# Kernel optimization log

Hardware: AMD Instinct MI355X
Metric: run time of the kernel (lower is better)

The kernel has to match this reference:

```python
import jax, jax.numpy as jnp
import numpy as np

QUANT_BLOCK = 32  # hardcoded in Linear8Bit


def setup_inputs() -> dict:
    key = jax.random.key(0)
    k1, k2, k3, k4, k5 = jax.random.split(key, 5)
    M, K, N = 64, 8192, 8192
    num_blocks = K // QUANT_BLOCK  # 256
    x = jax.random.normal(k1, (M, K), dtype=jnp.float32)
    scales = jax.random.uniform(k2, (num_blocks, N), dtype=jnp.float32, minval=0.001, maxval=0.02)
    zeros = jax.random.uniform(k3, (num_blocks, N), dtype=jnp.float32, minval=0.0, maxval=255.0)
    bias = jax.random.normal(k4, (N,), dtype=jnp.float32)
    quantized_weight = jax.random.randint(k5, (K, N), 0, 256, dtype=jnp.int32)
    return {"x": x, "scales": scales, "zeros": zeros, "bias": bias,
            "quantized_weight": quantized_weight}


def reference(x, scales, zeros, bias, quantized_weight):
    # The torch loop computes sum_b a_block @ (scale_b * (w_block - zero_b)),
    # which is exactly a full block-wise dequant followed by one matmul.
    K, N = quantized_weight.shape
    # Expand per-block scale/zero along K: [num_blocks, N] -> [K, N]
    scale_k = jnp.repeat(scales, QUANT_BLOCK, axis=0)[:K]
    zero_k = jnp.repeat(zeros, QUANT_BLOCK, axis=0)[:K]
    w_dq = scale_k * (quantized_weight.astype(jnp.float32) - zero_k)  # [K, N]
    out = jnp.matmul(x, w_dq) + bias  # [M, N]
    return out
```

## Files before the change

kernel.cpp:

```cpp
#include <hip/hip_runtime.h>

#define M_DIM 64
#define K_DIM 8192
#define N_DIM 8192
#define QB 32
#define NT 64
#define KC 64
#define SPLITS 4
#define KSPLIT (K_DIM / SPLITS)
#define NSTAGE (KSPLIT / KC)

typedef __attribute__((ext_vector_type(8))) short short8;
typedef __attribute__((ext_vector_type(8))) unsigned short ushort8;
typedef __attribute__((ext_vector_type(4))) float f32x4;
typedef __attribute__((ext_vector_type(4))) unsigned int u32x4;

static_assert(NSTAGE % 2 == 0 && NSTAGE * KC == KSPLIT, "tiling");

__device__ __forceinline__ unsigned short f2bf(float f) {
    unsigned u = __builtin_bit_cast(unsigned, f);
    u += 0x7fffu + ((u >> 16) & 1u);
    return (unsigned short)(u >> 16);
}

__global__ __launch_bounds__(256) void bias_init(const float* __restrict__ bias,
                                                 float* __restrict__ out) {
    int i = (blockIdx.x * 256 + threadIdx.x) * 4;
    *(f32x4*)(out + i) = *(const f32x4*)(bias + (i & (N_DIM - 1)));
}

__global__ __launch_bounds__(256) void xcvt(const float* __restrict__ x,
                                            unsigned short* __restrict__ xb) {
    int i = (blockIdx.x * 256 + threadIdx.x) * 8;
    f32x4 a = *(const f32x4*)(x + i);
    f32x4 b = *(const f32x4*)(x + i + 4);
    ushort8 o;
    #pragma unroll
    for (int e = 0; e < 4; ++e) { o[e] = f2bf(a[e]); o[4 + e] = f2bf(b[e]); }
    *(ushort8*)(xb + i) = o;
}

template <bool XBF>
__global__ __launch_bounds__(256, 2) void qgemm(
    const float* __restrict__ x,
    const unsigned short* __restrict__ xb,
    const float* __restrict__ scales,
    const float* __restrict__ zeros,
    const int*   __restrict__ qw,
    float*       __restrict__ out)
{
    __shared__ unsigned short lq[2][NT][72];
    __shared__ unsigned short lx[2][M_DIM][72];

    const int tid  = threadIdx.x;
    const int lane = tid & 63;
    const int w    = tid >> 6;

    const int n0 = blockIdx.x * NT;
    const int k0 = blockIdx.y * KSPLIT;

    const int qn   = n0 + lane;
    const int xrow = tid >> 2;
    const int xcol = (tid & 3) * 16;

    const int*   qp = qw     + (size_t)k0 * N_DIM + qn;
    const float* sp = scales + (size_t)(k0 >> 5) * N_DIM + qn;
    const float* zp = zeros  + (size_t)(k0 >> 5) * N_DIM + qn;

    int   qvA[16], qvB[16];
    float svA0, svA1, zvA0, zvA1, svB0, svB1, zvB0, zvB1;
    u32x4 xvA[2], xvB[2];
    f32x4 xfA[4], xfB[4];

#define LOADS(QV, S0, S1, Z0, Z1, XV, XF, T)                                  \
    do {                                                                      \
        const int* _p = qp + (size_t)(T) * KC * N_DIM;                        \
        _Pragma("unroll")                                                     \
        for (int s = 0; s < 4; ++s)                                           \
            _Pragma("unroll")                                                 \
            for (int j = 0; j < 4; ++j)                                       \
                QV[4 * s + j] = _p[(size_t)(16 * s + 4 * w + j) * N_DIM];     \
        S0 = sp[(size_t)(2 * (T)) * N_DIM];                                   \
        S1 = sp[(size_t)(2 * (T) + 1) * N_DIM];                               \
        Z0 = zp[(size_t)(2 * (T)) * N_DIM];                                   \
        Z1 = zp[(size_t)(2 * (T) + 1) * N_DIM];                               \
        if (XBF) {                                                            \
            const unsigned short* _xp =                                       \
                xb + (size_t)xrow * K_DIM + (k0 + (T) * KC) + xcol;           \
            XV[0] = *(const u32x4*)_xp;                                       \
            XV[1] = *(const u32x4*)(_xp + 8);                                 \
        } else {                                                              \
            const float* _xp =                                                \
                x + (size_t)xrow * K_DIM + (k0 + (T) * KC) + xcol;            \
            _Pragma("unroll")                                                 \
            for (int i = 0; i < 4; ++i) XF[i] = *(const f32x4*)(_xp + 4 * i); \
        }                                                                     \
    } while (0)

#define BODY(QV, S0, S1, Z0, Z1, XV, XF, CUR)                                 \
    do {                                                                      \
        const float _nz0 = -(S0) * (Z0), _nz1 = -(S1) * (Z1);                 \
        uint2 qd[4];                                                          \
        _Pragma("unroll")                                                     \
        for (int s = 0; s < 4; ++s) {                                         \
            const float _sc = (s < 2) ? (S0) : (S1);                          \
            const float _nz = (s < 2) ? _nz0 : _nz1;                          \
            unsigned short h0 = f2bf(fmaf((float)QV[4 * s + 0], _sc, _nz));   \
            unsigned short h1 = f2bf(fmaf((float)QV[4 * s + 1], _sc, _nz));   \
            unsigned short h2 = f2bf(fmaf((float)QV[4 * s + 2], _sc, _nz));   \
            unsigned short h3 = f2bf(fmaf((float)QV[4 * s + 3], _sc, _nz));   \
            qd[s].x = (unsigned)h0 | ((unsigned)h1 << 16);                    \
            qd[s].y = (unsigned)h2 | ((unsigned)h3 << 16);                    \
        }                                                                     \
        _Pragma("unroll")                                                     \
        for (int s = 0; s < 4; ++s)                                           \
            *(uint2*)&lq[CUR][lane][16 * s + 4 * w] = qd[s];                  \
        if (XBF) {                                                            \
            *(u32x4*)&lx[CUR][xrow][xcol]     = XV[0];                        \
            *(u32x4*)&lx[CUR][xrow][xcol + 8] = XV[1];                        \
        } else {                                                              \
            ushort8 xw0, xw1;                                                 \
            _Pragma("unroll")                                                 \
            for (int e = 0; e < 4; ++e) {                                     \
                xw0[e]     = f2bf(XF[0][e]);                                  \
                xw0[4 + e] = f2bf(XF[1][e]);                                  \
                xw1[e]     = f2bf(XF[2][e]);                                  \
                xw1[4 + e] = f2bf(XF[3][e]);                                  \
            }                                                                 \
            *(ushort8*)&lx[CUR][xrow][xcol]     = xw0;                        \
            *(ushort8*)&lx[CUR][xrow][xcol + 8] = xw1;                        \
        }                                                                     \
    } while (0)

#define MM(CUR)                                                               \
    do {                                                                      \
        _Pragma("unroll")                                                     \
        for (int c = 0; c < 2; ++c) {                                         \
            const short8 bf = *(const short8*)&lq[CUR][16 * w + (lane & 15)]  \
                                                 [32 * c + 8 * (lane >> 4)];  \
            _Pragma("unroll")                                                 \
            for (int r = 0; r < 4; ++r) {                                     \
                const short8 af = *(const short8*)&lx[CUR][16 * r + (lane & 15)] \
                                                     [32 * c + 8 * (lane >> 4)]; \
                acc[r] = __builtin_amdgcn_mfma_f32_16x16x32_bf16(af, bf, acc[r], 0, 0, 0); \
            }                                                                 \
        }                                                                     \
    } while (0)

    f32x4 acc[4];
    #pragma unroll
    for (int r = 0; r < 4; ++r) acc[r] = (f32x4){0.f, 0.f, 0.f, 0.f};

    LOADS(qvA, svA0, svA1, zvA0, zvA1, xvA, xfA, 0);

    for (int t = 0; t < NSTAGE; t += 2) {
        LOADS(qvB, svB0, svB1, zvB0, zvB1, xvB, xfB, t + 1);
        BODY(qvA, svA0, svA1, zvA0, zvA1, xvA, xfA, 0);
        __syncthreads();
        MM(0);
        if (t + 2 < NSTAGE)
            LOADS(qvA, svA0, svA1, zvA0, zvA1, xvA, xfA, t + 2);
        BODY(qvB, svB0, svB1, zvB0, zvB1, xvB, xfB, 1);
        __syncthreads();
        MM(1);
    }

#undef LOADS
#undef BODY
#undef MM

    const int cn = n0 + 16 * w + (lane & 15);
    #pragma unroll
    for (int r = 0; r < 4; ++r) {
        const int m = 16 * r + 4 * (lane >> 4);
        #pragma unroll
        for (int e = 0; e < 4; ++e)
            atomicAdd(out + (size_t)(m + e) * N_DIM + cn, acc[r][e]);
    }
}

extern "C" void kernel_launch(void* const* d_in, const int* in_sizes, int n_in,
                              void* d_out, int out_size, void* d_ws, size_t ws_size,
                              hipStream_t stream) {
    const float* x      = (const float*)d_in[0];
    const float* scales = (const float*)d_in[1];
    const float* zeros  = (const float*)d_in[2];
    const float* bias   = (const float*)d_in[3];
    const int*   qw     = (const int*)d_in[4];
    float* out = (float*)d_out;
    unsigned short* xbf = (unsigned short*)d_ws;

    const bool use_xbf = ws_size >= (size_t)M_DIM * K_DIM * 2;

    bias_init<<<dim3((M_DIM * N_DIM) / 1024), 256, 0, stream>>>(bias, out);
    if (use_xbf) {
        xcvt<<<dim3((M_DIM * K_DIM) / 2048), 256, 0, stream>>>(x, xbf);
        qgemm<true><<<dim3(N_DIM / NT, SPLITS), 256, 0, stream>>>(
            x, xbf, scales, zeros, qw, out);
    } else {
        qgemm<false><<<dim3(N_DIM / NT, SPLITS), 256, 0, stream>>>(
            x, nullptr, scales, zeros, qw, out);
    }
}
```

Before: 59.91 us.

## Deepen register prefetch to two stages ahead and use a raw LDS barrier

Global loads of quantized weights, scales, zeros and x are now issued two K-chunks ahead, using four rotating register sets instead of two. The loop is unrolled by four stages. Each __syncthreads is replaced by an explicit lgkmcnt(0) wait plus s_barrier, so the barrier no longer waits on the outstanding global prefetches. The aim is to keep more memory requests in flight on this bandwidth-bound dequant GEMM, at the cost of many more VGPRs and possibly lower occupancy.

```diff
diff --git a/kernel.cpp b/kernel.cpp
--- a/kernel.cpp
+++ b/kernel.cpp
@@ -15,7 +15,7 @@
 typedef __attribute__((ext_vector_type(4))) float f32x4;
 typedef __attribute__((ext_vector_type(4))) unsigned int u32x4;
 
-static_assert(NSTAGE % 2 == 0 && NSTAGE * KC == KSPLIT, "tiling");
+static_assert(NSTAGE % 4 == 0 && NSTAGE * KC == KSPLIT, "tiling");
 
 __device__ __forceinline__ unsigned short f2bf(float f) {
     unsigned u = __builtin_bit_cast(unsigned, f);
@@ -67,48 +67,49 @@
     const float* sp = scales + (size_t)(k0 >> 5) * N_DIM + qn;
     const float* zp = zeros  + (size_t)(k0 >> 5) * N_DIM + qn;
 
-    int   qvA[16], qvB[16];
-    float svA0, svA1, zvA0, zvA1, svB0, svB1, zvB0, zvB1;
-    u32x4 xvA[2], xvB[2];
-    f32x4 xfA[4], xfB[4];
-
-#define LOADS(QV, S0, S1, Z0, Z1, XV, XF, T)                                  \
+    int qv0[16], qv1[16], qv2[16], qv3[16];
+    float s0_0, s1_0, z0_0, z1_0, s0_1, s1_1, z0_1, z1_1;
+    float s0_2, s1_2, z0_2, z1_2, s0_3, s1_3, z0_3, z1_3;
+    u32x4 xv0[2], xv1[2], xv2[2], xv3[2];
+    f32x4 xf0[4], xf1[4], xf2[4], xf3[4];
+
+#define LOADS(S, T)                                                           \
     do {                                                                      \
         const int* _p = qp + (size_t)(T) * KC * N_DIM;                        \
         _Pragma("unroll")                                                     \
         for (int s = 0; s < 4; ++s)                                           \
             _Pragma("unroll")                                                 \
             for (int j = 0; j < 4; ++j)                                       \
-                QV[4 * s + j] = _p[(size_t)(16 * s + 4 * w + j) * N_DIM];     \
-        S0 = sp[(size_t)(2 * (T)) * N_DIM];                                   \
-        S1 = sp[(size_t)(2 * (T) + 1) * N_DIM];                               \
-        Z0 = zp[(size_t)(2 * (T)) * N_DIM];                                   \
-        Z1 = zp[(size_t)(2 * (T) + 1) * N_DIM];                               \
+                qv##S[4 * s + j] = _p[(size_t)(16 * s + 4 * w + j) * N_DIM];  \
+        s0_##S = sp[(size_t)(2 * (T)) * N_DIM];                               \
+        s1_##S = sp[(size_t)(2 * (T) + 1) * N_DIM];                           \
+        z0_##S = zp[(size_t)(2 * (T)) * N_DIM];                               \
+        z1_##S = zp[(size_t)(2 * (T) + 1) * N_DIM];                           \
         if (XBF) {                                                            \
             const unsigned short* _xp =                                       \
                 xb + (size_t)xrow * K_DIM + (k0 + (T) * KC) + xcol;           \
-            XV[0] = *(const u32x4*)_xp;                                       \
-            XV[1] = *(const u32x4*)(_xp + 8);                                 \
+            xv##S[0] = *(const u32x4*)_xp;                                    \
+            xv##S[1] = *(const u32x4*)(_xp + 8);                              \
         } else {                                                              \
             const float* _xp =                                                \
                 x + (size_t)xrow * K_DIM + (k0 + (T) * KC) + xcol;            \
             _Pragma("unroll")                                                 \
-            for (int i = 0; i < 4; ++i) XF[i] = *(const f32x4*)(_xp + 4 * i); \
-        }                                                                     \
-    } while (0)
-
-#define BODY(QV, S0, S1, Z0, Z1, XV, XF, CUR)                                 \
-    do {                                                                      \
-        const float _nz0 = -(S0) * (Z0), _nz1 = -(S1) * (Z1);                 \
+            for (int i = 0; i < 4; ++i) xf##S[i] = *(const f32x4*)(_xp + 4 * i); \
+        }                                                                     \
+    } while (0)
+
+#define BODY(S, CUR)                                                          \
+    do {                                                                      \
+        const float _nz0 = -s0_##S * z0_##S, _nz1 = -s1_##S * z1_##S;         \
         uint2 qd[4];                                                          \
         _Pragma("unroll")                                                     \
         for (int s = 0; s < 4; ++s) {                                         \
-            const float _sc = (s < 2) ? (S0) : (S1);                          \
+            const float _sc = (s < 2) ? s0_##S : s1_##S;                      \
             const float _nz = (s < 2) ? _nz0 : _nz1;                          \
-            unsigned short h0 = f2bf(fmaf((float)QV[4 * s + 0], _sc, _nz));   \
-            unsigned short h1 = f2bf(fmaf((float)QV[4 * s + 1], _sc, _nz));   \
-            unsigned short h2 = f2bf(fmaf((float)QV[4 * s + 2], _sc, _nz));   \
-            unsigned short h3 = f2bf(fmaf((float)QV[4 * s + 3], _sc, _nz));   \
+            unsigned short h0 = f2bf(fmaf((float)qv##S[4 * s + 0], _sc, _nz)); \
+            unsigned short h1 = f2bf(fmaf((float)qv##S[4 * s + 1], _sc, _nz)); \
+            unsigned short h2 = f2bf(fmaf((float)qv##S[4 * s + 2], _sc, _nz)); \
+            unsigned short h3 = f2bf(fmaf((float)qv##S[4 * s + 3], _sc, _nz)); \
             qd[s].x = (unsigned)h0 | ((unsigned)h1 << 16);                    \
             qd[s].y = (unsigned)h2 | ((unsigned)h3 << 16);                    \
         }                                                                     \
@@ -116,16 +117,16 @@
         for (int s = 0; s < 4; ++s)                                           \
             *(uint2*)&lq[CUR][lane][16 * s + 4 * w] = qd[s];                  \
         if (XBF) {                                                            \
-            *(u32x4*)&lx[CUR][xrow][xcol]     = XV[0];                        \
-            *(u32x4*)&lx[CUR][xrow][xcol + 8] = XV[1];                        \
+            *(u32x4*)&lx[CUR][xrow][xcol]     = xv##S[0];                     \
+            *(u32x4*)&lx[CUR][xrow][xcol + 8] = xv##S[1];                     \
         } else {                                                              \
             ushort8 xw0, xw1;                                                 \
             _Pragma("unroll")                                                 \
             for (int e = 0; e < 4; ++e) {                                     \
-                xw0[e]     = f2bf(XF[0][e]);                                  \
-                xw0[4 + e] = f2bf(XF[1][e]);                                  \
-                xw1[e]     = f2bf(XF[2][e]);                                  \
-                xw1[4 + e] = f2bf(XF[3][e]);                                  \
+                xw0[e]     = f2bf(xf##S[0][e]);                               \
+                xw0[4 + e] = f2bf(xf##S[1][e]);                               \
+                xw1[e]     = f2bf(xf##S[2][e]);                               \
+                xw1[4 + e] = f2bf(xf##S[3][e]);                               \
             }                                                                 \
             *(ushort8*)&lx[CUR][xrow][xcol]     = xw0;                        \
             *(ushort8*)&lx[CUR][xrow][xcol + 8] = xw1;                        \
@@ -147,27 +148,33 @@
         }                                                                     \
     } while (0)
 
+#define STAGE(S, P, T, CUR)                                                   \
+    do {                                                                      \
+        if ((T) + 2 < NSTAGE) LOADS(P, (T) + 2);                              \
+        BODY(S, CUR);                                                         \
+        asm volatile("s_waitcnt lgkmcnt(0)" ::: "memory");                    \
+        __builtin_amdgcn_s_barrier();                                         \
+        MM(CUR);                                                              \
+    } while (0)
+
     f32x4 acc[4];
     #pragma unroll
     for (int r = 0; r < 4; ++r) acc[r] = (f32x4){0.f, 0.f, 0.f, 0.f};
 
-    LOADS(qvA, svA0, svA1, zvA0, zvA1, xvA, xfA, 0);
-
-    for (int t = 0; t < NSTAGE; t += 2) {
-        LOADS(qvB, svB0, svB1, zvB0, zvB1, xvB, xfB, t + 1);
-        BODY(qvA, svA0, svA1, zvA0, zvA1, xvA, xfA, 0);
-        __syncthreads();
-        MM(0);
-        if (t + 2 < NSTAGE)
-            LOADS(qvA, svA0, svA1, zvA0, zvA1, xvA, xfA, t + 2);
-        BODY(qvB, svB0, svB1, zvB0, zvB1, xvB, xfB, 1);
-        __syncthreads();
-        MM(1);
+    LOADS(0, 0);
+    LOADS(1, 1);
+
+    for (int t = 0; t < NSTAGE; t += 4) {
+        STAGE(0, 2, t + 0, 0);
+        STAGE(1, 3, t + 1, 1);
+        STAGE(2, 0, t + 2, 0);
+        STAGE(3, 1, t + 3, 1);
     }
 
 #undef LOADS
 #undef BODY
 #undef MM
+#undef STAGE
 
     const int cn = n0 + 16 * w + (lane & 15);
     #pragma unroll
```

Measured after the change: 60.66 us. Within noise of the previous version (+1.3%).

## Widen N tile with vectorized int4 weight loads, raise split-K, fuse prep kernels

Applied to the files above, without the earlier changes.

Restructures the quantized GEMM so each block covers 256 output columns with K chunks of 32. Each thread now loads int32x4 weight vectors along N and writes the dequantized values transposed into LDS. Each wave computes a 4x4 grid of MFMA tiles, and split-K rises to 16 so the grid keeps enough blocks. The x-to-bf16 conversion and bias initialization are merged into one prep launch to save a kernel launch. In exchange, the kernel uses more accumulator registers and performs four times as many atomic adds to the output.

```diff
diff --git a/kernel.cpp b/kernel.cpp
--- a/kernel.cpp
+++ b/kernel.cpp
@@ -4,15 +4,16 @@
 #define K_DIM 8192
 #define N_DIM 8192
 #define QB 32
-#define NT 64
-#define KC 64
-#define SPLITS 4
+#define NT 256
+#define KC 32
+#define SPLITS 16
 #define KSPLIT (K_DIM / SPLITS)
 #define NSTAGE (KSPLIT / KC)
 
 typedef __attribute__((ext_vector_type(8))) short short8;
 typedef __attribute__((ext_vector_type(8))) unsigned short ushort8;
 typedef __attribute__((ext_vector_type(4))) float f32x4;
+typedef __attribute__((ext_vector_type(4))) int i32x4;
 typedef __attribute__((ext_vector_type(4))) unsigned int u32x4;
 
 static_assert(NSTAGE % 2 == 0 && NSTAGE * KC == KSPLIT, "tiling");
@@ -23,21 +24,29 @@
     return (unsigned short)(u >> 16);
 }
 
+__global__ __launch_bounds__(256) void prep(const float* __restrict__ x,
+                                            unsigned short* __restrict__ xb,
+                                            const float* __restrict__ bias,
+                                            float* __restrict__ out) {
+    const int b = blockIdx.x;
+    if (b < 256) {
+        int i = (b * 256 + threadIdx.x) * 8;
+        f32x4 a = *(const f32x4*)(x + i);
+        f32x4 c = *(const f32x4*)(x + i + 4);
+        ushort8 o;
+        #pragma unroll
+        for (int e = 0; e < 4; ++e) { o[e] = f2bf(a[e]); o[4 + e] = f2bf(c[e]); }
+        *(ushort8*)(xb + i) = o;
+    } else {
+        int i = ((b - 256) * 256 + threadIdx.x) * 4;
+        *(f32x4*)(out + i) = *(const f32x4*)(bias + (i & (N_DIM - 1)));
+    }
+}
+
 __global__ __launch_bounds__(256) void bias_init(const float* __restrict__ bias,
                                                  float* __restrict__ out) {
     int i = (blockIdx.x * 256 + threadIdx.x) * 4;
     *(f32x4*)(out + i) = *(const f32x4*)(bias + (i & (N_DIM - 1)));
-}
-
-__global__ __launch_bounds__(256) void xcvt(const float* __restrict__ x,
-                                            unsigned short* __restrict__ xb) {
-    int i = (blockIdx.x * 256 + threadIdx.x) * 8;
-    f32x4 a = *(const f32x4*)(x + i);
-    f32x4 b = *(const f32x4*)(x + i + 4);
-    ushort8 o;
-    #pragma unroll
-    for (int e = 0; e < 4; ++e) { o[e] = f2bf(a[e]); o[4 + e] = f2bf(b[e]); }
-    *(ushort8*)(xb + i) = o;
 }
 
 template <bool XBF>
@@ -49,118 +58,111 @@
     const int*   __restrict__ qw,
     float*       __restrict__ out)
 {
-    __shared__ unsigned short lq[2][NT][72];
-    __shared__ unsigned short lx[2][M_DIM][72];
+    __shared__ unsigned short lw[2][NT][40];
+    __shared__ unsigned short lx[2][M_DIM][40];
 
     const int tid  = threadIdx.x;
     const int lane = tid & 63;
     const int w    = tid >> 6;
+    const int q    = lane >> 4;
+    const int lm   = lane & 15;
 
     const int n0 = blockIdx.x * NT;
     const int k0 = blockIdx.y * KSPLIT;
 
-    const int qn   = n0 + lane;
+    const int*   qp = qw     + (size_t)k0 * N_DIM        + n0 + 4 * lane;
+    const float* sp = scales + (size_t)(k0 >> 5) * N_DIM + n0 + 4 * lane;
+    const float* zp = zeros  + (size_t)(k0 >> 5) * N_DIM + n0 + 4 * lane;
+
     const int xrow = tid >> 2;
-    const int xcol = (tid & 3) * 16;
-
-    const int*   qp = qw     + (size_t)k0 * N_DIM + qn;
-    const float* sp = scales + (size_t)(k0 >> 5) * N_DIM + qn;
-    const float* zp = zeros  + (size_t)(k0 >> 5) * N_DIM + qn;
-
-    int   qvA[16], qvB[16];
-    float svA0, svA1, zvA0, zvA1, svB0, svB1, zvB0, zvB1;
-    u32x4 xvA[2], xvB[2];
-    f32x4 xfA[4], xfB[4];
-
-#define LOADS(QV, S0, S1, Z0, Z1, XV, XF, T)                                  \
+    const int xq   = tid & 3;
+
+    i32x4 qvA[8], qvB[8];
+    f32x4 scA, zcA, scB, zcB;
+    u32x4 xvA, xvB;
+    f32x4 xfA[2], xfB[2];
+
+#define LOADS(S, T)                                                           \
     do {                                                                      \
         const int* _p = qp + (size_t)(T) * KC * N_DIM;                        \
         _Pragma("unroll")                                                     \
-        for (int s = 0; s < 4; ++s)                                           \
-            _Pragma("unroll")                                                 \
-            for (int j = 0; j < 4; ++j)                                       \
-                QV[4 * s + j] = _p[(size_t)(16 * s + 4 * w + j) * N_DIM];     \
-        S0 = sp[(size_t)(2 * (T)) * N_DIM];                                   \
-        S1 = sp[(size_t)(2 * (T) + 1) * N_DIM];                               \
-        Z0 = zp[(size_t)(2 * (T)) * N_DIM];                                   \
-        Z1 = zp[(size_t)(2 * (T) + 1) * N_DIM];                               \
+        for (int i = 0; i < 8; ++i)                                           \
+            qv##S[i] = *(const i32x4*)(_p + (size_t)(8 * w + i) * N_DIM);     \
+        sc##S = *(const f32x4*)(sp + (size_t)(T) * N_DIM);                    \
+        zc##S = *(const f32x4*)(zp + (size_t)(T) * N_DIM);                    \
         if (XBF) {                                                            \
-            const unsigned short* _xp =                                       \
-                xb + (size_t)xrow * K_DIM + (k0 + (T) * KC) + xcol;           \
-            XV[0] = *(const u32x4*)_xp;                                       \
-            XV[1] = *(const u32x4*)(_xp + 8);                                 \
+            xv##S = *(const u32x4*)(xb + (size_t)xrow * K_DIM                 \
+                                    + (k0 + (T) * KC) + 8 * xq);              \
         } else {                                                              \
-            const float* _xp =                                                \
-                x + (size_t)xrow * K_DIM + (k0 + (T) * KC) + xcol;            \
-            _Pragma("unroll")                                                 \
-            for (int i = 0; i < 4; ++i) XF[i] = *(const f32x4*)(_xp + 4 * i); \
+            const float* _xp = x + (size_t)xrow * K_DIM                       \
+                                 + (k0 + (T) * KC) + 8 * xq;                  \
+            xf##S[0] = *(const f32x4*)_xp;                                    \
+            xf##S[1] = *(const f32x4*)(_xp + 4);                              \
         }                                                                     \
     } while (0)
 
-#define BODY(QV, S0, S1, Z0, Z1, XV, XF, CUR)                                 \
+#define BODY(S, CUR)                                                          \
     do {                                                                      \
-        const float _nz0 = -(S0) * (Z0), _nz1 = -(S1) * (Z1);                 \
-        uint2 qd[4];                                                          \
-        _Pragma("unroll")                                                     \
-        for (int s = 0; s < 4; ++s) {                                         \
-            const float _sc = (s < 2) ? (S0) : (S1);                          \
-            const float _nz = (s < 2) ? _nz0 : _nz1;                          \
-            unsigned short h0 = f2bf(fmaf((float)QV[4 * s + 0], _sc, _nz));   \
-            unsigned short h1 = f2bf(fmaf((float)QV[4 * s + 1], _sc, _nz));   \
-            unsigned short h2 = f2bf(fmaf((float)QV[4 * s + 2], _sc, _nz));   \
-            unsigned short h3 = f2bf(fmaf((float)QV[4 * s + 3], _sc, _nz));   \
-            qd[s].x = (unsigned)h0 | ((unsigned)h1 << 16);                    \
-            qd[s].y = (unsigned)h2 | ((unsigned)h3 << 16);                    \
+        const f32x4 _nz = -sc##S * zc##S;                                     \
+        _Pragma("unroll")                                                     \
+        for (int j = 0; j < 3 + 1; ++j) {                                     \
+            unsigned hh[4];                                                   \
+            _Pragma("unroll")                                                 \
+            for (int p = 0; p < 4; ++p) {                                     \
+                unsigned short h0 =                                           \
+                    f2bf(fmaf((float)qv##S[2 * p][j],     sc##S[j], _nz[j])); \
+                unsigned short h1 =                                           \
+                    f2bf(fmaf((float)qv##S[2 * p + 1][j], sc##S[j], _nz[j])); \
+                hh[p] = (unsigned)h0 | ((unsigned)h1 << 16);                  \
+            }                                                                 \
+            *(u32x4*)&lw[CUR][4 * lane + j][8 * w] =                          \
+                (u32x4){hh[0], hh[1], hh[2], hh[3]};                          \
         }                                                                     \
-        _Pragma("unroll")                                                     \
-        for (int s = 0; s < 4; ++s)                                           \
-            *(uint2*)&lq[CUR][lane][16 * s + 4 * w] = qd[s];                  \
         if (XBF) {                                                            \
-            *(u32x4*)&lx[CUR][xrow][xcol]     = XV[0];                        \
-            *(u32x4*)&lx[CUR][xrow][xcol + 8] = XV[1];                        \
+            *(u32x4*)&lx[CUR][xrow][8 * xq] = xv##S;                          \
         } else {                                                              \
-            ushort8 xw0, xw1;                                                 \
+            ushort8 xw;                                                       \
             _Pragma("unroll")                                                 \
             for (int e = 0; e < 4; ++e) {                                     \
-                xw0[e]     = f2bf(XF[0][e]);                                  \
-                xw0[4 + e] = f2bf(XF[1][e]);                                  \
-                xw1[e]     = f2bf(XF[2][e]);                                  \
-                xw1[4 + e] = f2bf(XF[3][e]);                                  \
+                xw[e]     = f2bf(xf##S[0][e]);                                \
+                xw[4 + e] = f2bf(xf##S[1][e]);                                \
             }                                                                 \
-            *(ushort8*)&lx[CUR][xrow][xcol]     = xw0;                        \
-            *(ushort8*)&lx[CUR][xrow][xcol + 8] = xw1;                        \
+            *(ushort8*)&lx[CUR][xrow][8 * xq] = xw;                           \
         }                                                                     \
     } while (0)
 
 #define MM(CUR)                                                               \
     do {                                                                      \
-        _Pragma("unroll")                                                     \
-        for (int c = 0; c < 2; ++c) {                                         \
-            const short8 bf = *(const short8*)&lq[CUR][16 * w + (lane & 15)]  \
-                                                 [32 * c + 8 * (lane >> 4)];  \
+        short8 bf[4], af[4];                                                  \
+        _Pragma("unroll")                                                     \
+        for (int g = 0; g < 4; ++g)                                           \
+            bf[g] = *(const short8*)&lw[CUR][64 * w + 16 * g + lm][8 * q];    \
+        _Pragma("unroll")                                                     \
+        for (int r = 0; r < 4; ++r)                                           \
+            af[r] = *(const short8*)&lx[CUR][16 * r + lm][8 * q];             \
+        _Pragma("unroll")                                                     \
+        for (int g = 0; g < 4; ++g)                                           \
             _Pragma("unroll")                                                 \
-            for (int r = 0; r < 4; ++r) {                                     \
-                const short8 af = *(const short8*)&lx[CUR][16 * r + (lane & 15)] \
-                                                     [32 * c + 8 * (lane >> 4)]; \
-                acc[r] = __builtin_amdgcn_mfma_f32_16x16x32_bf16(af, bf, acc[r], 0, 0, 0); \
-            }                                                                 \
-        }                                                                     \
+            for (int r = 0; r < 4; ++r)                                       \
+                acc[g][r] = __builtin_amdgcn_mfma_f32_16x16x32_bf16(          \
+                    af[r], bf[g], acc[g][r], 0, 0, 0);                        \
     } while (0)
 
-    f32x4 acc[4];
+    f32x4 acc[4][4];
     #pragma unroll
-    for (int r = 0; r < 4; ++r) acc[r] = (f32x4){0.f, 0.f, 0.f, 0.f};
-
-    LOADS(qvA, svA0, svA1, zvA0, zvA1, xvA, xfA, 0);
+    for (int a = 0; a < 4; ++a)
+        #pragma unroll
+        for (int b = 0; b < 4; ++b) acc[a][b] = (f32x4){0.f, 0.f, 0.f, 0.f};
+
+    LOADS(A, 0);
 
     for (int t = 0; t < NSTAGE; t += 2) {
-        LOADS(qvB, svB0, svB1, zvB0, zvB1, xvB, xfB, t + 1);
-        BODY(qvA, svA0, svA1, zvA0, zvA1, xvA, xfA, 0);
+        LOADS(B, t + 1);
+        BODY(A, 0);
         __syncthreads();
         MM(0);
-        if (t + 2 < NSTAGE)
-            LOADS(qvA, svA0, svA1, zvA0, zvA1, xvA, xfA, t + 2);
-        BODY(qvB, svB0, svB1, zvB0, zvB1, xvB, xfB, 1);
+        if (t + 2 < NSTAGE) LOADS(A, t + 2);
+        BODY(B, 1);
         __syncthreads();
         MM(1);
     }
@@ -169,13 +171,16 @@
 #undef BODY
 #undef MM
 
-    const int cn = n0 + 16 * w + (lane & 15);
     #pragma unroll
-    for (int r = 0; r < 4; ++r) {
-        const int m = 16 * r + 4 * (lane >> 4);
+    for (int g = 0; g < 4; ++g) {
+        const int cn = n0 + 64 * w + 16 * g + lm;
         #pragma unroll
-        for (int e = 0; e < 4; ++e)
-            atomicAdd(out + (size_t)(m + e) * N_DIM + cn, acc[r][e]);
+        for (int r = 0; r < 4; ++r) {
+            const int m = 16 * r + 4 * q;
+            #pragma unroll
+            for (int e = 0; e < 4; ++e)
+                atomicAdd(out + (size_t)(m + e) * N_DIM + cn, acc[g][r][e]);
+        }
     }
 }
 
@@ -192,12 +197,12 @@
 
     const bool use_xbf = ws_size >= (size_t)M_DIM * K_DIM * 2;
 
-    bias_init<<<dim3((M_DIM * N_DIM) / 1024), 256, 0, stream>>>(bias, out);
     if (use_xbf) {
-        xcvt<<<dim3((M_DIM * K_DIM) / 2048), 256, 0, stream>>>(x, xbf);
+        prep<<<dim3(768), 256, 0, stream>>>(x, xbf, bias, out);
         qgemm<true><<<dim3(N_DIM / NT, SPLITS), 256, 0, stream>>>(
             x, xbf, scales, zeros, qw, out);
     } else {
+        bias_init<<<dim3((M_DIM * N_DIM) / 1024), 256, 0, stream>>>(bias, out);
         qgemm<false><<<dim3(N_DIM / NT, SPLITS), 256, 0, stream>>>(
             x, nullptr, scales, zeros, qw, out);
     }
```

Measured after the change: 76.34 us. 27.4% more time.
